# Kernel tuning notes

Hardware: AMD Instinct MI355X
Metric: run time of the kernel (lower is better)

## Reference

```python
import jax, jax.numpy as jnp
import numpy as np

CUTOFF = 5.0

def cubic_cutoff(d):
    # f(0)=1, f(y)=0, smooth first derivatives at both ends
    y = CUTOFF
    xc = 1.0 - 1.5 * (d * d) / (y * y) + 0.5 * (d * d * d) / (y * y * y)
    return jnp.where(d <= 0.0, 1.0, jnp.where(d >= y, 0.0, xc))


def setup_inputs() -> dict:
    key = jax.random.key(0)
    ks = jax.random.split(key, 16)
    B, N, H = 64, 64, 128
    h = jax.random.normal(ks[0], (B, N, H), jnp.float32)
    x = jax.random.uniform(ks[1], (B, N, 3), jnp.float32) * 10.0  # 10A box -> partial neighbor sparsity
    node_mask = jnp.ones((B, N), dtype=bool)
    h0 = jax.random.normal(ks[2], (B, N, H), jnp.float32)
    s = lambda fin: 1.0 / np.sqrt(fin)
    # edge_mlp: Linear(2H+1 -> H), SiLU, Linear(H -> H), SiLU
    We1 = jax.random.normal(ks[3], (2 * H + 1, H), jnp.float32) * s(2 * H + 1)
    be1 = jnp.zeros((H,), jnp.float32)
    We2 = jax.random.normal(ks[4], (H, H), jnp.float32) * s(H)
    be2 = jnp.zeros((H,), jnp.float32)
    # node_mlp: Linear(H + residual_nf + H = 3H -> H), SiLU, Linear(H -> H)
    Wn1 = jax.random.normal(ks[5], (3 * H, H), jnp.float32) * s(3 * H)
    bn1 = jnp.zeros((H,), jnp.float32)
    Wn2 = jax.random.normal(ks[6], (H, H), jnp.float32) * s(H)
    bn2 = jnp.zeros((H,), jnp.float32)
    # coord_mlp: Linear(H -> H), SiLU, Linear(H -> 1, no bias, xavier gain=0.001)
    Wc1 = jax.random.normal(ks[7], (H, H), jnp.float32) * s(H)
    bc1 = jnp.zeros((H,), jnp.float32)
    Wc2 = jax.random.normal(ks[8], (H, 1), jnp.float32) * (0.001 * s(H))
    return {"h": h, "x": x, "node_mask": node_mask, "h0": h0,
            "We1": We1, "be1": be1, "We2": We2, "be2": be2,
            "Wn1": Wn1, "bn1": bn1, "Wn2": Wn2, "bn2": bn2,
            "Wc1": Wc1, "bc1": bc1, "Wc2": Wc2}


def reference(h, x, node_mask, h0, We1, be1, We2, be2, Wn1, bn1, Wn2, bn2, Wc1, bc1, Wc2):
    B, N, H = h.shape
    # pairwise distances; distances are detached in the torch default path
    diff = x[:, :, None, :] - x[:, None, :, :]                     # [B,N,N,3]
    d = jax.lax.stop_gradient(jnp.sqrt(jnp.sum(diff * diff, -1)))  # [B,N,N]
    eye = jnp.eye(N, dtype=bool)[None]
    mask = (node_mask[:, :, None] & node_mask[:, None, :]
            & (d < CUTOFF) & (~eye))                               # [B,N,N]
    maskf = mask.astype(h.dtype)
    # edge model: feat[b,j,k] = [h[b,j], h[b,k], d^2]
    feat = jnp.concatenate([
        jnp.broadcast_to(h[:, :, None, :], (B, N, N, H)),
        jnp.broadcast_to(h[:, None, :, :], (B, N, N, H)),
        (d * d)[..., None]], axis=-1)                              # [B,N,N,2H+1]
    e = jax.nn.silu(feat @ We1 + be1)
    e = jax.nn.silu(e @ We2 + be2)
    mij = e * (cubic_cutoff(d) * maskf)[..., None]                 # [B,N,N,H]
    # node model: sum messages into receiver j
    mi = jnp.sum(mij, axis=2)                                      # [B,N,H]
    nfeat = jnp.concatenate([h, mi, h0], axis=-1)                  # [B,N,3H]
    h_out = jax.nn.silu(nfeat @ Wn1 + bn1) @ Wn2 + bn2
    h_new = h + h_out                                              # recurrent
    # coord model (scatter-add semantics of the intended math)
    phi = jax.nn.silu(mij @ Wc1 + bc1) @ Wc2                       # [B,N,N,1]
    C = 1.0 / (N - 1.0)
    x_up = C * jnp.sum(diff * phi * maskf[..., None], axis=2)      # [B,N,3]
    x_new = jnp.clip(x + x_up, -1000.0, 1000.0)
    return (h_new, x_new)
```

## Files before the change

kernel.cpp:

```cpp
#include <hip/hip_runtime.h>

#define Hh 128
#define Nn 64
#define CAP 2048
#define TPB 16

typedef _Float16 f16x8 __attribute__((ext_vector_type(8)));
typedef float f32x4 __attribute__((ext_vector_type(4)));
typedef unsigned int u32;

__device__ __forceinline__ float silu_f(float v){
    return v * __builtin_amdgcn_rcpf(1.0f + __expf(-v));
}
__device__ __forceinline__ int swz(int row, int cb){ return row*256 + (cb ^ ((row & 7) << 4)); }

#define WT_BYTES (9*32768)

__global__ __launch_bounds__(256) void k_wp(
    const float* __restrict__ x,
    const float* __restrict__ We1, const float* __restrict__ We2, const float* __restrict__ Wc1,
    const float* __restrict__ Wn1, const float* __restrict__ Wn2, char* __restrict__ wT,
    u32* __restrict__ cntB, u32* __restrict__ off_g, u32* __restrict__ cnt_g,
    u32* __restrict__ code_g, float* __restrict__ d2_g, float* __restrict__ cut_g)
{
    const int tid = threadIdx.x;
    if (blockIdx.x >= 64){
        if (blockIdx.x == 128){
            if (tid < 16){
                f16x8 v;
                #pragma unroll
                for (int i=0;i<8;i++) v[i] = (_Float16)We1[256*Hh + tid*8 + i];
                *(f16x8*)(wT + 8*32768 + tid*16) = v;
            }
            return;
        }
        const int id  = (blockIdx.x-64)*256 + tid;
        const int mat = id >> 11;
        const int r   = id & 2047;
        const int n   = r >> 4;
        const int kg  = r & 15;
        const float* __restrict__ src;
        int koff = 0;
        switch (mat){
            case 0: src = We2; break;
            case 1: src = Wc1; break;
            case 2: src = Wn1; break;
            case 3: src = Wn1; koff = 128; break;
            case 4: src = Wn1; koff = 256; break;
            case 5: src = Wn2; break;
            case 6: src = We1; break;
            default: src = We1; koff = 128; break;
        }
        f16x8 v;
        #pragma unroll
        for (int i=0;i<8;i++) v[i] = (_Float16)src[(koff + kg*8 + i)*Hh + n];
        *(f16x8*)(wT + mat*32768 + n*256 + kg*16) = v;
        return;
    }

    __shared__ float sX[192];
    __shared__ int sCnt[64], sOff[64];
    const int b  = blockIdx.x;
    const int wd = tid >> 6;
    const int l  = tid & 63;

    if (tid < 192) sX[tid] = x[b*192 + tid];
    __syncthreads();

    for (int jj = 0; jj < 16; jj++){
        const int j = wd*16 + jj;
        const float dx0 = sX[j*3+0]-sX[l*3+0];
        const float dx1 = sX[j*3+1]-sX[l*3+1];
        const float dx2 = sX[j*3+2]-sX[l*3+2];
        const float d2 = dx0*dx0 + dx1*dx1 + dx2*dx2;
        const bool valid = (l != j) && (d2 < 25.0f);
        const unsigned long long bal = __ballot(valid);
        if (l == 0) sCnt[j] = (int)__popcll(bal);
    }
    __syncthreads();
    if (tid < 64){
        int v = sCnt[tid];
        int incl = v;
        #pragma unroll
        for (int off=1; off<64; off<<=1){
            int o = __shfl_up(incl, off);
            if (l >= off) incl += o;
        }
        sOff[tid] = incl - v;
    }
    __syncthreads();
    if (tid < 64){
        off_g[b*64 + tid] = (u32)sOff[tid];
        cnt_g[b*64 + tid] = (u32)sCnt[tid];
        if (tid == 63){
            int tot = sOff[63] + sCnt[63];
            cntB[b] = (u32)(tot > CAP ? CAP : tot);
        }
    }
    for (int jj = 0; jj < 16; jj++){
        const int j = wd*16 + jj;
        const float dx0 = sX[j*3+0]-sX[l*3+0];
        const float dx1 = sX[j*3+1]-sX[l*3+1];
        const float dx2 = sX[j*3+2]-sX[l*3+2];
        const float d2 = dx0*dx0 + dx1*dx1 + dx2*dx2;
        const bool valid = (l != j) && (d2 < 25.0f);
        const unsigned long long bal = __ballot(valid);
        const int pos = __popcll(bal & ((1ull << l) - 1ull));
        if (valid){
            const int dst = sOff[j] + pos;
            if (dst < CAP){
                const int e = b*CAP + dst;
                code_g[e] = (u32)((j << 6) | l);
                d2_g[e]   = d2;
                cut_g[e]  = 1.0f - 0.06f*d2 + 0.004f*d2*sqrtf(d2);
            }
        }
    }
}

__global__ __launch_bounds__(256, 2) void k_preG(
    const float* __restrict__ h, const char* __restrict__ wT, const float* __restrict__ be1,
    _Float16* __restrict__ Aout, _Float16* __restrict__ Bout)
{
    __shared__ __align__(16) char sA[4096];

    const int r0  = blockIdx.x * 16;
    const int tid = threadIdx.x;
    const int w   = tid >> 6;
    const int l   = tid & 63;
    const int lrow= l & 15;
    const int lk  = l >> 4;
    const int n0 = 2*w, n1 = n0 + 1;
    const int colA = n0*16 + lrow, colB = n1*16 + lrow;

    {
        const int row = tid >> 4;
        const int g   = tid & 15;
        const float4* src = (const float4*)(h + (r0+row)*Hh + g*8);
        const float4 v0 = src[0], v1 = src[1];
        f16x8 e;
        e[0]=(_Float16)v0.x; e[1]=(_Float16)v0.y; e[2]=(_Float16)v0.z; e[3]=(_Float16)v0.w;
        e[4]=(_Float16)v1.x; e[5]=(_Float16)v1.y; e[6]=(_Float16)v1.z; e[7]=(_Float16)v1.w;
        *(f16x8*)(sA + swz(row, g*16)) = e;
    }
    __syncthreads();

    const char* WaT = wT + 6*32768;
    const char* WbT = wT + 7*32768;

    f32x4 accA[2], accB[2];
    {
        const float ba = be1[colA], bb = be1[colB];
        accA[0] = (f32x4){ba,ba,ba,ba};
        accA[1] = (f32x4){bb,bb,bb,bb};
        accB[0] = (f32x4){0.f,0.f,0.f,0.f};
        accB[1] = (f32x4){0.f,0.f,0.f,0.f};
    }
    #pragma unroll
    for (int kb=0;kb<4;kb++){
        const int cb = kb*64 + lk*16;
        const f16x8 a   = *(const f16x8*)(sA  + swz(lrow, cb));
        const f16x8 bA0 = *(const f16x8*)(WaT + (n0*16+lrow)*256 + cb);
        const f16x8 bA1 = *(const f16x8*)(WaT + (n1*16+lrow)*256 + cb);
        const f16x8 bB0 = *(const f16x8*)(WbT + (n0*16+lrow)*256 + cb);
        const f16x8 bB1 = *(const f16x8*)(WbT + (n1*16+lrow)*256 + cb);
        accA[0] = __builtin_amdgcn_mfma_f32_16x16x32_f16(a, bA0, accA[0], 0, 0, 0);
        accA[1] = __builtin_amdgcn_mfma_f32_16x16x32_f16(a, bA1, accA[1], 0, 0, 0);
        accB[0] = __builtin_amdgcn_mfma_f32_16x16x32_f16(a, bB0, accB[0], 0, 0, 0);
        accB[1] = __builtin_amdgcn_mfma_f32_16x16x32_f16(a, bB1, accB[1], 0, 0, 0);
    }
    #pragma unroll
    for (int r=0;r<4;r++){
        const int row = r0 + lk*4 + r;
        Aout[row*Hh + colA] = (_Float16)accA[0][r];
        Aout[row*Hh + colB] = (_Float16)accA[1][r];
        Bout[row*Hh + colA] = (_Float16)accB[0][r];
        Bout[row*Hh + colB] = (_Float16)accB[1][r];
    }
}

__global__ __launch_bounds__(256, 2) void k_edge(
    const _Float16* __restrict__ Ain, const _Float16* __restrict__ Bin,
    const char* __restrict__ wT,
    const float* __restrict__ be2_g, const float* __restrict__ bc1_g, const float* __restrict__ Wc2,
    const u32* __restrict__ cntB, const u32* __restrict__ code_g,
    const float* __restrict__ d2_g, const float* __restrict__ cut_g,
    float* __restrict__ mi_p, float* __restrict__ phi_g)
{
    __shared__ __align__(16) char sE1[32768];
    __shared__ __align__(16) char sM[32768];
    __shared__ int   sBj[128];
    __shared__ u32   sCode[128];
    __shared__ float sD2[128], sCut[128];
    __shared__ float sPhP[4][128];

    const int bid = blockIdx.x;
    const int b   = bid & 63;
    const int t   = bid >> 6;
    const int E_b = (int)cntB[b];
    const int r0  = t*128;
    if (r0 >= E_b) return;
    const int R   = (E_b - r0 < 128) ? (E_b - r0) : 128;
    const int MT  = (R + 15) >> 4;

    const int tid = threadIdx.x;
    const int w   = tid >> 6;
    const int l   = tid & 63;
    const int lrow= l & 15;
    const int lk  = l >> 4;
    const int n0 = 2*w, n1 = n0 + 1;
    const int colA = n0*16 + lrow, colB = n1*16 + lrow;
    const char* We2T = wT;
    const char* Wc1T = wT + 32768;

    if (tid < 128){
        if (tid < R){
            const u32 c = code_g[b*CAP + r0 + tid];
            sCode[tid] = c;
            sBj[tid]   = (int)(c >> 6);
            sD2[tid]   = d2_g[b*CAP + r0 + tid];
            sCut[tid]  = cut_g[b*CAP + r0 + tid];
        } else {
            sCode[tid] = 0; sBj[tid] = -1; sD2[tid] = 0.f; sCut[tid] = 0.f;
        }
    }
    __syncthreads();

    {
        const f16x8* W6 = (const f16x8*)(wT + 8*32768);
        #pragma unroll
        for (int pass=0; pass<2; pass++){
            const int row = pass*64 + (tid >> 2);
            if (row < MT*16){
                const int q = tid & 3;
                const u32 c = sCode[row];
                const int jl = (int)(c >> 6), kl = (int)(c & 63);
                const _Float16 d2h = (_Float16)sD2[row];
                f16x8 dsplat;
                #pragma unroll
                for (int i=0;i<8;i++) dsplat[i] = d2h;
                const f16x8* Aj = (const f16x8*)(Ain + (b*Nn+jl)*Hh + q*32);
                const f16x8* Bk = (const f16x8*)(Bin + (b*Nn+kl)*Hh + q*32);
                #pragma unroll
                for (int s=0;s<4;s++){
                    f16x8 pre = Aj[s] + Bk[s] + W6[q*4+s]*dsplat;
                    f16x8 e;
                    #pragma unroll
                    for (int i=0;i<8;i++) e[i] = (_Float16)silu_f((float)pre[i]);
                    *(f16x8*)(sE1 + swz(row, q*64 + s*16)) = e;
                }
            }
        }
    }
    __syncthreads();

    f32x4 acc[4][2];
    for (int tb = 0; tb < MT; tb += 4){
        const int MTp = (MT - tb < 4) ? (MT - tb) : 4;
        {
            const float b2a = be2_g[colA], b2b = be2_g[colB];
            #pragma unroll
            for (int mt=0;mt<4;mt++){
                acc[mt][0] = (f32x4){b2a,b2a,b2a,b2a};
                acc[mt][1] = (f32x4){b2b,b2b,b2b,b2b};
            }
        }
        #pragma unroll
        for (int kb=0;kb<4;kb++){
            const int cb = kb*64 + lk*16;
            const f16x8 bA = *(const f16x8*)(We2T + (n0*16+lrow)*256 + cb);
            const f16x8 bB = *(const f16x8*)(We2T + (n1*16+lrow)*256 + cb);
            #pragma unroll
            for (int mt=0;mt<4;mt++){
                if (mt < MTp){
                    const f16x8 a = *(const f16x8*)(sE1 + swz((tb+mt)*16 + lrow, cb));
                    acc[mt][0] = __builtin_amdgcn_mfma_f32_16x16x32_f16(a, bA, acc[mt][0], 0, 0, 0);
                    acc[mt][1] = __builtin_amdgcn_mfma_f32_16x16x32_f16(a, bB, acc[mt][1], 0, 0, 0);
                }
            }
        }
        #pragma unroll
        for (int mt=0;mt<4;mt++){
            if (mt < MTp){
                #pragma unroll
                for (int r=0;r<4;r++){
                    const int row = (tb+mt)*16 + lk*4 + r;
                    const float m0 = silu_f(acc[mt][0][r]) * sCut[row];
                    const float m1 = silu_f(acc[mt][1][r]) * sCut[row];
                    const int xr  = (row & 7) << 4;
                    *(_Float16*)(sM + row*256 + ((colA*2) ^ xr)) = (_Float16)m0;
                    *(_Float16*)(sM + row*256 + ((colB*2) ^ xr)) = (_Float16)m1;
                }
            }
        }
    }
    __syncthreads();

    for (int tb = 0; tb < MT; tb += 4){
        const int MTp = (MT - tb < 4) ? (MT - tb) : 4;
        {
            const float c1a = bc1_g[colA], c1b = bc1_g[colB];
            #pragma unroll
            for (int mt=0;mt<4;mt++){
                acc[mt][0] = (f32x4){c1a,c1a,c1a,c1a};
                acc[mt][1] = (f32x4){c1b,c1b,c1b,c1b};
            }
        }
        #pragma unroll
        for (int kb=0;kb<4;kb++){
            const int cb = kb*64 + lk*16;
            const f16x8 bA = *(const f16x8*)(Wc1T + (n0*16+lrow)*256 + cb);
            const f16x8 bB = *(const f16x8*)(Wc1T + (n1*16+lrow)*256 + cb);
            #pragma unroll
            for (int mt=0;mt<4;mt++){
                if (mt < MTp){
                    const f16x8 a = *(const f16x8*)(sM + swz((tb+mt)*16 + lrow, cb));
                    acc[mt][0] = __builtin_amdgcn_mfma_f32_16x16x32_f16(a, bA, acc[mt][0], 0, 0, 0);
                    acc[mt][1] = __builtin_amdgcn_mfma_f32_16x16x32_f16(a, bB, acc[mt][1], 0, 0, 0);
                }
            }
        }
        const float wca = Wc2[colA], wcb = Wc2[colB];
        float php[16];
        #pragma unroll
        for (int mt=0;mt<4;mt++){
            if (mt < MTp){
                #pragma unroll
                for (int r=0;r<4;r++)
                    php[mt*4+r] = silu_f(acc[mt][0][r])*wca + silu_f(acc[mt][1][r])*wcb;
            }
        }
        #pragma unroll
        for (int i=0;i<16;i++){
            if ((i>>2) < MTp){
                php[i] += __shfl_xor(php[i], 1);
                php[i] += __shfl_xor(php[i], 2);
                php[i] += __shfl_xor(php[i], 4);
                php[i] += __shfl_xor(php[i], 8);
            }
        }
        if (lrow == 0){
            #pragma unroll
            for (int mt=0;mt<4;mt++){
                if (mt < MTp){
                    #pragma unroll
                    for (int r=0;r<4;r++)
                        sPhP[w][(tb+mt)*16 + lk*4 + r] = php[mt*4+r];
                }
            }
        }
    }

    {
        const int col  = tid & 127;
        const int half = tid >> 7;
        const int slot = (t & 1)*2 + half;
        float sum = 0.f;
        int cur = -1;
        const int rbeg = half*64, rend = rbeg + 64;
        for (int r = rbeg; r < rend; ++r){
            const int bj = sBj[r];
            const float m = (float)(*(const _Float16*)(sM + r*256 + ((col*2) ^ ((r&7)<<4))));
            if (bj != cur){
                if (cur >= 0) mi_p[((size_t)slot*4096 + (b<<6) + cur)*128 + col] = sum;
                cur = bj; sum = 0.f;
            }
            sum += m;
        }
        if (cur >= 0) mi_p[((size_t)slot*4096 + (b<<6) + cur)*128 + col] = sum;
    }
    __syncthreads();

    if (tid < 128 && tid < R){
        const float phi = sPhP[0][tid] + sPhP[1][tid] + sPhP[2][tid] + sPhP[3][tid];
        phi_g[b*CAP + r0 + tid] = phi;
    }
}

__global__ __launch_bounds__(256) void k_reduce(
    const float* __restrict__ x,
    const u32* __restrict__ off_g, const u32* __restrict__ cnt_g,
    const u32* __restrict__ code_g, const float* __restrict__ phi_g,
    const float* __restrict__ mi_p,
    _Float16* __restrict__ mi_g, float* __restrict__ out_x)
{
    const int tid = threadIdx.x;
    const int wd  = tid >> 6;
    const int l   = tid & 63;
    const int gid = blockIdx.x*4 + wd;
    const int b   = gid >> 6;

    const int cnt = (int)cnt_g[gid];
    const int off = (int)off_g[gid];

    bool v0=false, v1=false, v2=false, v3=false;
    if (cnt > 0){
        const int t0 = off >> 7;
        const int t1 = (off + cnt - 1) >> 7;
        {
            const int s0 = off - t0*128;
            const int e0 = ((off+cnt) < (t0+1)*128 ? (off+cnt) : (t0+1)*128) - t0*128;
            const bool h0 = (s0 < 64), h1 = (e0 > 64);
            if ((t0 & 1) == 0){ v0 |= h0; v1 |= h1; } else { v2 |= h0; v3 |= h1; }
        }
        if (t1 != t0){
            const int e0 = (off + cnt) - t1*128;
            const bool h0 = true, h1 = (e0 > 64);
            if ((t1 & 1) == 0){ v0 |= h0; v1 |= h1; } else { v2 |= h0; v3 |= h1; }
        }
    }

    #pragma unroll
    for (int p=0;p<2;p++){
        const int col = l*2 + p;
        const size_t base = (size_t)gid*128 + col;
        float s = 0.f;
        if (v0) s += mi_p[base];
        if (v1) s += mi_p[(size_t)4096*128 + base];
        if (v2) s += mi_p[(size_t)2*4096*128 + base];
        if (v3) s += mi_p[(size_t)3*4096*128 + base];
        mi_g[gid*Hh + col] = (_Float16)s;
    }

    float w0=0.f, w1=0.f, w2=0.f;
    if (l < cnt && (off + l) < CAP){
        const int e = b*CAP + off + l;
        const int kl = (int)(code_g[e] & 63);
        const float phi = phi_g[e];
        w0 = (x[gid*3+0] - x[(b*Nn+kl)*3+0]) * phi;
        w1 = (x[gid*3+1] - x[(b*Nn+kl)*3+1]) * phi;
        w2 = (x[gid*3+2] - x[(b*Nn+kl)*3+2]) * phi;
    }
    #pragma unroll
    for (int off2=1; off2<64; off2<<=1){
        w0 += __shfl_xor(w0, off2);
        w1 += __shfl_xor(w1, off2);
        w2 += __shfl_xor(w2, off2);
    }
    if (l == 0){
        const float C = 1.0f/63.0f;
        out_x[gid*3+0] = fminf(fmaxf(x[gid*3+0] + C*w0, -1000.f), 1000.f);
        out_x[gid*3+1] = fminf(fmaxf(x[gid*3+1] + C*w1, -1000.f), 1000.f);
        out_x[gid*3+2] = fminf(fmaxf(x[gid*3+2] + C*w2, -1000.f), 1000.f);
    }
}

__global__ __launch_bounds__(256, 2) void k_node(
    const float* __restrict__ h, const _Float16* __restrict__ mi_g,
    const float* __restrict__ h0,
    const char* __restrict__ wT,
    const float* __restrict__ bn1_g, const float* __restrict__ bn2_g,
    float* __restrict__ out_h)
{
    __shared__ __align__(16) char sA[8192];
    __shared__ __align__(16) char sHid[8192];

    const int r0  = blockIdx.x * 32;
    const int tid = threadIdx.x;
    const int w   = tid >> 6;
    const int l   = tid & 63;
    const int lrow= l & 15;
    const int lk  = l >> 4;
    const int n0 = 2*w, n1 = n0 + 1;
    const int colA = n0*16 + lrow, colB = n1*16 + lrow;

    f32x4 acc[2][2];
    {
        const float b1a = bn1_g[colA], b1b = bn1_g[colB];
        acc[0][0] = (f32x4){b1a,b1a,b1a,b1a};
        acc[0][1] = (f32x4){b1b,b1b,b1b,b1b};
        acc[1][0] = (f32x4){b1a,b1a,b1a,b1a};
        acc[1][1] = (f32x4){b1b,b1b,b1b,b1b};
    }

    const int arow = tid >> 3;
    const int g    = tid & 7;

    for (int c = 0; c < 3; c++){
        if (c == 1){
            const f16x8* src = (const f16x8*)(mi_g + (r0+arow)*Hh + g*16);
            *(f16x8*)(sA + swz(arow, g*32))      = src[0];
            *(f16x8*)(sA + swz(arow, g*32+16))   = src[1];
        } else {
            const float* base = (c == 0) ? h : h0;
            const float4* src = (const float4*)(base + (r0+arow)*Hh + g*16);
            const float4 v0=src[0], v1=src[1], v2=src[2], v3=src[3];
            f16x8 e0, e1;
            e0[0]=(_Float16)v0.x; e0[1]=(_Float16)v0.y; e0[2]=(_Float16)v0.z; e0[3]=(_Float16)v0.w;
            e0[4]=(_Float16)v1.x; e0[5]=(_Float16)v1.y; e0[6]=(_Float16)v1.z; e0[7]=(_Float16)v1.w;
            e1[0]=(_Float16)v2.x; e1[1]=(_Float16)v2.y; e1[2]=(_Float16)v2.z; e1[3]=(_Float16)v2.w;
            e1[4]=(_Float16)v3.x; e1[5]=(_Float16)v3.y; e1[6]=(_Float16)v3.z; e1[7]=(_Float16)v3.w;
            *(f16x8*)(sA + swz(arow, g*32))    = e0;
            *(f16x8*)(sA + swz(arow, g*32+16)) = e1;
        }
        __syncthreads();
        const char* Wimg = wT + (2+c)*32768;
        #pragma unroll
        for (int kb=0;kb<4;kb++){
            const int cb = kb*64 + lk*16;
            const f16x8 bA = *(const f16x8*)(Wimg + (n0*16+lrow)*256 + cb);
            const f16x8 bB = *(const f16x8*)(Wimg + (n1*16+lrow)*256 + cb);
            #pragma unroll
            for (int mt=0;mt<2;mt++){
                const f16x8 a = *(const f16x8*)(sA + swz(mt*16 + lrow, cb));
                acc[mt][0] = __builtin_amdgcn_mfma_f32_16x16x32_f16(a, bA, acc[mt][0], 0, 0, 0);
                acc[mt][1] = __builtin_amdgcn_mfma_f32_16x16x32_f16(a, bB, acc[mt][1], 0, 0, 0);
            }
        }
        __syncthreads();
    }

    #pragma unroll
    for (int mt=0;mt<2;mt++){
        #pragma unroll
        for (int r=0;r<4;r++){
            const int row = mt*16 + lk*4 + r;
            const int xr  = (row & 7) << 4;
            *(_Float16*)(sHid + row*256 + ((colA*2) ^ xr)) = (_Float16)silu_f(acc[mt][0][r]);
            *(_Float16*)(sHid + row*256 + ((colB*2) ^ xr)) = (_Float16)silu_f(acc[mt][1][r]);
        }
    }
    __syncthreads();

    const char* Wn2T = wT + 5*32768;
    f32x4 acc2[2][2];
    {
        const float b2a = bn2_g[colA], b2b = bn2_g[colB];
        acc2[0][0] = (f32x4){b2a,b2a,b2a,b2a};
        acc2[0][1] = (f32x4){b2b,b2b,b2b,b2b};
        acc2[1][0] = (f32x4){b2a,b2a,b2a,b2a};
        acc2[1][1] = (f32x4){b2b,b2b,b2b,b2b};
    }
    #pragma unroll
    for (int kb=0;kb<4;kb++){
        const int cb = kb*64 + lk*16;
        const f16x8 bA = *(const f16x8*)(Wn2T + (n0*16+lrow)*256 + cb);
        const f16x8 bB = *(const f16x8*)(Wn2T + (n1*16+lrow)*256 + cb);
        #pragma unroll
        for (int mt=0;mt<2;mt++){
            const f16x8 a = *(const f16x8*)(sHid + swz(mt*16 + lrow, cb));
            acc2[mt][0] = __builtin_amdgcn_mfma_f32_16x16x32_f16(a, bA, acc2[mt][0], 0, 0, 0);
            acc2[mt][1] = __builtin_amdgcn_mfma_f32_16x16x32_f16(a, bB, acc2[mt][1], 0, 0, 0);
        }
    }
    #pragma unroll
    for (int mt=0;mt<2;mt++){
        #pragma unroll
        for (int r=0;r<4;r++){
            const int row = r0 + mt*16 + lk*4 + r;
            out_h[row*Hh + colA] = h[row*Hh + colA] + acc2[mt][0][r];
            out_h[row*Hh + colB] = h[row*Hh + colB] + acc2[mt][1][r];
        }
    }
}

extern "C" void kernel_launch(void* const* d_in, const int* in_sizes, int n_in,
                              void* d_out, int out_size, void* d_ws, size_t ws_size,
                              hipStream_t stream) {
    const float* h   = (const float*)d_in[0];
    const float* x   = (const float*)d_in[1];
    const float* h0  = (const float*)d_in[3];
    const float* We1 = (const float*)d_in[4];
    const float* be1 = (const float*)d_in[5];
    const float* We2 = (const float*)d_in[6];
    const float* be2 = (const float*)d_in[7];
    const float* Wn1 = (const float*)d_in[8];
    const float* bn1 = (const float*)d_in[9];
    const float* Wn2 = (const float*)d_in[10];
    const float* bn2 = (const float*)d_in[11];
    const float* Wc1 = (const float*)d_in[12];
    const float* bc1 = (const float*)d_in[13];
    const float* Wc2 = (const float*)d_in[14];

    float* out_h = (float*)d_out;
    float* out_x = out_h + 64*64*128;

    char*      wT   = (char*)d_ws;
    _Float16*  A    = (_Float16*)(wT + WT_BYTES);
    _Float16*  Bv   = A + 4096*128;
    _Float16*  mi   = Bv + 4096*128;
    u32*       cntB = (u32*)(mi + 4096*128);
    u32*       offg = cntB + 64;
    u32*       cntg = offg + 4096;
    u32*       code = cntg + 4096;
    float*     d2g  = (float*)(code + 64*CAP);
    float*     cutg = d2g + 64*CAP;
    float*     phig = cutg + 64*CAP;
    float*     mip  = phig + 64*CAP;

    k_wp    <<<129, 256, 0, stream>>>(x, We1, We2, Wc1, Wn1, Wn2, wT,
                                      cntB, offg, cntg, code, d2g, cutg);
    k_preG  <<<256, 256, 0, stream>>>(h, wT, be1, A, Bv);
    k_edge  <<<64*TPB, 256, 0, stream>>>(A, Bv, wT, be2, bc1, Wc2,
                                         cntB, code, d2g, cutg, mip, phig);
    k_reduce<<<1024, 256, 0, stream>>>(x, offg, cntg, code, phig, mip, mi, out_x);
    k_node  <<<128, 256, 0, stream>>>(h, mi, h0, wT, bn1, bn2, out_h);
}
```

Measured before the change: 83.57 us.

## Drop reduce kernel: fold coord update into edge, partial sums into node

The k_reduce launch is removed. The edge kernel now computes per-receiver coordinate partial sums directly from stored dx vectors and phi. The node kernel merges the mi partials and x_up partials using a slot mask. Edge tiles shrink from 128 to 64 rows with twice as many blocks, which raises parallelism and halves shared memory per block. This saves one launch and the phi round trip, at the cost of extra global reads of fp32 partials inside k_node.

```diff
diff --git a/kernel.cpp b/kernel.cpp
--- a/kernel.cpp
+++ b/kernel.cpp
@@ -3,7 +3,7 @@
 #define Hh 128
 #define Nn 64
 #define CAP 2048
-#define TPB 16
+#define TPB 32
 
 typedef _Float16 f16x8 __attribute__((ext_vector_type(8)));
 typedef float f32x4 __attribute__((ext_vector_type(4)));
@@ -13,6 +13,25 @@
     return v * __builtin_amdgcn_rcpf(1.0f + __expf(-v));
 }
 __device__ __forceinline__ int swz(int row, int cb){ return row*256 + (cb ^ ((row & 7) << 4)); }
+
+__device__ __forceinline__ int slot_mask(int off, int cnt){
+    if (cnt <= 0) return 0;
+    const int t0 = off >> 6, t1 = (off + cnt - 1) >> 6;
+    const int s0 = off & 63;
+    const int lim = (t0 + 1) << 6;
+    const int end0 = ((off + cnt) < lim ? (off + cnt) : lim) - (t0 << 6);
+    int m = 0;
+    const int p0 = (t0 & 1) * 2;
+    if (s0 < 32)   m |= 1 << p0;
+    if (end0 > 32) m |= 1 << (p0 + 1);
+    if (t1 != t0){
+        const int e1 = (off + cnt) - (t1 << 6);
+        const int p1 = (t1 & 1) * 2;
+        m |= 1 << p1;
+        if (e1 > 32) m |= 1 << (p1 + 1);
+    }
+    return m;
+}
 
 #define WT_BYTES (9*32768)
 
@@ -21,7 +40,7 @@
     const float* __restrict__ We1, const float* __restrict__ We2, const float* __restrict__ Wc1,
     const float* __restrict__ Wn1, const float* __restrict__ Wn2, char* __restrict__ wT,
     u32* __restrict__ cntB, u32* __restrict__ off_g, u32* __restrict__ cnt_g,
-    u32* __restrict__ code_g, float* __restrict__ d2_g, float* __restrict__ cut_g)
+    u32* __restrict__ code_g, float4* __restrict__ dx_g, float* __restrict__ cut_g)
 {
     const int tid = threadIdx.x;
     if (blockIdx.x >= 64){
@@ -111,7 +130,7 @@
             if (dst < CAP){
                 const int e = b*CAP + dst;
                 code_g[e] = (u32)((j << 6) | l);
-                d2_g[e]   = d2;
+                dx_g[e]   = (float4){dx0, dx1, dx2, d2};
                 cut_g[e]  = 1.0f - 0.06f*d2 + 0.004f*d2*sqrtf(d2);
             }
         }
@@ -184,23 +203,24 @@
     const char* __restrict__ wT,
     const float* __restrict__ be2_g, const float* __restrict__ bc1_g, const float* __restrict__ Wc2,
     const u32* __restrict__ cntB, const u32* __restrict__ code_g,
-    const float* __restrict__ d2_g, const float* __restrict__ cut_g,
-    float* __restrict__ mi_p, float* __restrict__ phi_g)
+    const float4* __restrict__ dx_g, const float* __restrict__ cut_g,
+    float* __restrict__ mi_p, float* __restrict__ xup_p)
 {
-    __shared__ __align__(16) char sE1[32768];
-    __shared__ __align__(16) char sM[32768];
-    __shared__ int   sBj[128];
-    __shared__ u32   sCode[128];
-    __shared__ float sD2[128], sCut[128];
-    __shared__ float sPhP[4][128];
+    __shared__ __align__(16) char sE1[16384];
+    __shared__ __align__(16) char sM[16384];
+    __shared__ int    sBj[64];
+    __shared__ u32    sCode[64];
+    __shared__ float4 sDxD[64];
+    __shared__ float  sCut[64];
+    __shared__ float  sPhP[4][64];
 
     const int bid = blockIdx.x;
     const int b   = bid & 63;
     const int t   = bid >> 6;
     const int E_b = (int)cntB[b];
-    const int r0  = t*128;
+    const int r0  = t*64;
     if (r0 >= E_b) return;
-    const int R   = (E_b - r0 < 128) ? (E_b - r0) : 128;
+    const int R   = (E_b - r0 < 64) ? (E_b - r0) : 64;
     const int MT  = (R + 15) >> 4;
 
     const int tid = threadIdx.x;
@@ -213,57 +233,53 @@
     const char* We2T = wT;
     const char* Wc1T = wT + 32768;
 
-    if (tid < 128){
+    if (tid < 64){
         if (tid < R){
             const u32 c = code_g[b*CAP + r0 + tid];
             sCode[tid] = c;
             sBj[tid]   = (int)(c >> 6);
-            sD2[tid]   = d2_g[b*CAP + r0 + tid];
+            sDxD[tid]  = dx_g[b*CAP + r0 + tid];
             sCut[tid]  = cut_g[b*CAP + r0 + tid];
         } else {
-            sCode[tid] = 0; sBj[tid] = -1; sD2[tid] = 0.f; sCut[tid] = 0.f;
+            sCode[tid] = 0; sBj[tid] = -1;
+            sDxD[tid]  = (float4){0.f,0.f,0.f,0.f};
+            sCut[tid]  = 0.f;
         }
     }
     __syncthreads();
 
     {
         const f16x8* W6 = (const f16x8*)(wT + 8*32768);
-        #pragma unroll
-        for (int pass=0; pass<2; pass++){
-            const int row = pass*64 + (tid >> 2);
-            if (row < MT*16){
-                const int q = tid & 3;
-                const u32 c = sCode[row];
-                const int jl = (int)(c >> 6), kl = (int)(c & 63);
-                const _Float16 d2h = (_Float16)sD2[row];
-                f16x8 dsplat;
+        const int row = tid >> 2;
+        if (row < MT*16){
+            const int q = tid & 3;
+            const u32 c = sCode[row];
+            const int jl = (int)(c >> 6), kl = (int)(c & 63);
+            const _Float16 d2h = (_Float16)sDxD[row].w;
+            f16x8 dsplat;
+            #pragma unroll
+            for (int i=0;i<8;i++) dsplat[i] = d2h;
+            const f16x8* Aj = (const f16x8*)(Ain + (b*Nn+jl)*Hh + q*32);
+            const f16x8* Bk = (const f16x8*)(Bin + (b*Nn+kl)*Hh + q*32);
+            #pragma unroll
+            for (int s=0;s<4;s++){
+                f16x8 pre = Aj[s] + Bk[s] + W6[q*4+s]*dsplat;
+                f16x8 e;
                 #pragma unroll
-                for (int i=0;i<8;i++) dsplat[i] = d2h;
-                const f16x8* Aj = (const f16x8*)(Ain + (b*Nn+jl)*Hh + q*32);
-                const f16x8* Bk = (const f16x8*)(Bin + (b*Nn+kl)*Hh + q*32);
-                #pragma unroll
-                for (int s=0;s<4;s++){
-                    f16x8 pre = Aj[s] + Bk[s] + W6[q*4+s]*dsplat;
-                    f16x8 e;
-                    #pragma unroll
-                    for (int i=0;i<8;i++) e[i] = (_Float16)silu_f((float)pre[i]);
-                    *(f16x8*)(sE1 + swz(row, q*64 + s*16)) = e;
-                }
+                for (int i=0;i<8;i++) e[i] = (_Float16)silu_f((float)pre[i]);
+                *(f16x8*)(sE1 + swz(row, q*64 + s*16)) = e;
             }
         }
     }
     __syncthreads();
 
     f32x4 acc[4][2];
-    for (int tb = 0; tb < MT; tb += 4){
-        const int MTp = (MT - tb < 4) ? (MT - tb) : 4;
-        {
-            const float b2a = be2_g[colA], b2b = be2_g[colB];
-            #pragma unroll
-            for (int mt=0;mt<4;mt++){
-                acc[mt][0] = (f32x4){b2a,b2a,b2a,b2a};
-                acc[mt][1] = (f32x4){b2b,b2b,b2b,b2b};
-            }
+    {
+        const float b2a = be2_g[colA], b2b = be2_g[colB];
+        #pragma unroll
+        for (int mt=0;mt<4;mt++){
+            acc[mt][0] = (f32x4){b2a,b2a,b2a,b2a};
+            acc[mt][1] = (f32x4){b2b,b2b,b2b,b2b};
         }
         #pragma unroll
         for (int kb=0;kb<4;kb++){
@@ -272,8 +288,8 @@
             const f16x8 bB = *(const f16x8*)(We2T + (n1*16+lrow)*256 + cb);
             #pragma unroll
             for (int mt=0;mt<4;mt++){
-                if (mt < MTp){
-                    const f16x8 a = *(const f16x8*)(sE1 + swz((tb+mt)*16 + lrow, cb));
+                if (mt < MT){
+                    const f16x8 a = *(const f16x8*)(sE1 + swz(mt*16 + lrow, cb));
                     acc[mt][0] = __builtin_amdgcn_mfma_f32_16x16x32_f16(a, bA, acc[mt][0], 0, 0, 0);
                     acc[mt][1] = __builtin_amdgcn_mfma_f32_16x16x32_f16(a, bB, acc[mt][1], 0, 0, 0);
                 }
@@ -281,10 +297,10 @@
         }
         #pragma unroll
         for (int mt=0;mt<4;mt++){
-            if (mt < MTp){
+            if (mt < MT){
                 #pragma unroll
                 for (int r=0;r<4;r++){
-                    const int row = (tb+mt)*16 + lk*4 + r;
+                    const int row = mt*16 + lk*4 + r;
                     const float m0 = silu_f(acc[mt][0][r]) * sCut[row];
                     const float m1 = silu_f(acc[mt][1][r]) * sCut[row];
                     const int xr  = (row & 7) << 4;
@@ -296,15 +312,12 @@
     }
     __syncthreads();
 
-    for (int tb = 0; tb < MT; tb += 4){
-        const int MTp = (MT - tb < 4) ? (MT - tb) : 4;
-        {
-            const float c1a = bc1_g[colA], c1b = bc1_g[colB];
-            #pragma unroll
-            for (int mt=0;mt<4;mt++){
-                acc[mt][0] = (f32x4){c1a,c1a,c1a,c1a};
-                acc[mt][1] = (f32x4){c1b,c1b,c1b,c1b};
-            }
+    {
+        const float c1a = bc1_g[colA], c1b = bc1_g[colB];
+        #pragma unroll
+        for (int mt=0;mt<4;mt++){
+            acc[mt][0] = (f32x4){c1a,c1a,c1a,c1a};
+            acc[mt][1] = (f32x4){c1b,c1b,c1b,c1b};
         }
         #pragma unroll
         for (int kb=0;kb<4;kb++){
@@ -313,8 +326,8 @@
             const f16x8 bB = *(const f16x8*)(Wc1T + (n1*16+lrow)*256 + cb);
             #pragma unroll
             for (int mt=0;mt<4;mt++){
-                if (mt < MTp){
-                    const f16x8 a = *(const f16x8*)(sM + swz((tb+mt)*16 + lrow, cb));
+                if (mt < MT){
+                    const f16x8 a = *(const f16x8*)(sM + swz(mt*16 + lrow, cb));
                     acc[mt][0] = __builtin_amdgcn_mfma_f32_16x16x32_f16(a, bA, acc[mt][0], 0, 0, 0);
                     acc[mt][1] = __builtin_amdgcn_mfma_f32_16x16x32_f16(a, bB, acc[mt][1], 0, 0, 0);
                 }
@@ -324,7 +337,7 @@
         float php[16];
         #pragma unroll
         for (int mt=0;mt<4;mt++){
-            if (mt < MTp){
+            if (mt < MT){
                 #pragma unroll
                 for (int r=0;r<4;r++)
                     php[mt*4+r] = silu_f(acc[mt][0][r])*wca + silu_f(acc[mt][1][r])*wcb;
@@ -332,7 +345,7 @@
         }
         #pragma unroll
         for (int i=0;i<16;i++){
-            if ((i>>2) < MTp){
+            if ((i>>2) < MT){
                 php[i] += __shfl_xor(php[i], 1);
                 php[i] += __shfl_xor(php[i], 2);
                 php[i] += __shfl_xor(php[i], 4);
@@ -342,10 +355,10 @@
         if (lrow == 0){
             #pragma unroll
             for (int mt=0;mt<4;mt++){
-                if (mt < MTp){
+                if (mt < MT){
                     #pragma unroll
                     for (int r=0;r<4;r++)
-                        sPhP[w][(tb+mt)*16 + lk*4 + r] = php[mt*4+r];
+                        sPhP[w][mt*16 + lk*4 + r] = php[mt*4+r];
                 }
             }
         }
@@ -357,7 +370,7 @@
         const int slot = (t & 1)*2 + half;
         float sum = 0.f;
         int cur = -1;
-        const int rbeg = half*64, rend = rbeg + 64;
+        const int rbeg = half*32, rend = rbeg + 32;
         for (int r = rbeg; r < rend; ++r){
             const int bj = sBj[r];
             const float m = (float)(*(const _Float16*)(sM + r*256 + ((col*2) ^ ((r&7)<<4))));
@@ -371,86 +384,35 @@
     }
     __syncthreads();
 
-    if (tid < 128 && tid < R){
-        const float phi = sPhP[0][tid] + sPhP[1][tid] + sPhP[2][tid] + sPhP[3][tid];
-        phi_g[b*CAP + r0 + tid] = phi;
-    }
-}
-
-__global__ __launch_bounds__(256) void k_reduce(
-    const float* __restrict__ x,
-    const u32* __restrict__ off_g, const u32* __restrict__ cnt_g,
-    const u32* __restrict__ code_g, const float* __restrict__ phi_g,
-    const float* __restrict__ mi_p,
-    _Float16* __restrict__ mi_g, float* __restrict__ out_x)
-{
-    const int tid = threadIdx.x;
-    const int wd  = tid >> 6;
-    const int l   = tid & 63;
-    const int gid = blockIdx.x*4 + wd;
-    const int b   = gid >> 6;
-
-    const int cnt = (int)cnt_g[gid];
-    const int off = (int)off_g[gid];
-
-    bool v0=false, v1=false, v2=false, v3=false;
-    if (cnt > 0){
-        const int t0 = off >> 7;
-        const int t1 = (off + cnt - 1) >> 7;
-        {
-            const int s0 = off - t0*128;
-            const int e0 = ((off+cnt) < (t0+1)*128 ? (off+cnt) : (t0+1)*128) - t0*128;
-            const bool h0 = (s0 < 64), h1 = (e0 > 64);
-            if ((t0 & 1) == 0){ v0 |= h0; v1 |= h1; } else { v2 |= h0; v3 |= h1; }
-        }
-        if (t1 != t0){
-            const int e0 = (off + cnt) - t1*128;
-            const bool h0 = true, h1 = (e0 > 64);
-            if ((t1 & 1) == 0){ v0 |= h0; v1 |= h1; } else { v2 |= h0; v3 |= h1; }
-        }
-    }
-
-    #pragma unroll
-    for (int p=0;p<2;p++){
-        const int col = l*2 + p;
-        const size_t base = (size_t)gid*128 + col;
-        float s = 0.f;
-        if (v0) s += mi_p[base];
-        if (v1) s += mi_p[(size_t)4096*128 + base];
-        if (v2) s += mi_p[(size_t)2*4096*128 + base];
-        if (v3) s += mi_p[(size_t)3*4096*128 + base];
-        mi_g[gid*Hh + col] = (_Float16)s;
-    }
-
-    float w0=0.f, w1=0.f, w2=0.f;
-    if (l < cnt && (off + l) < CAP){
-        const int e = b*CAP + off + l;
-        const int kl = (int)(code_g[e] & 63);
-        const float phi = phi_g[e];
-        w0 = (x[gid*3+0] - x[(b*Nn+kl)*3+0]) * phi;
-        w1 = (x[gid*3+1] - x[(b*Nn+kl)*3+1]) * phi;
-        w2 = (x[gid*3+2] - x[(b*Nn+kl)*3+2]) * phi;
-    }
-    #pragma unroll
-    for (int off2=1; off2<64; off2<<=1){
-        w0 += __shfl_xor(w0, off2);
-        w1 += __shfl_xor(w1, off2);
-        w2 += __shfl_xor(w2, off2);
-    }
-    if (l == 0){
-        const float C = 1.0f/63.0f;
-        out_x[gid*3+0] = fminf(fmaxf(x[gid*3+0] + C*w0, -1000.f), 1000.f);
-        out_x[gid*3+1] = fminf(fmaxf(x[gid*3+1] + C*w1, -1000.f), 1000.f);
-        out_x[gid*3+2] = fminf(fmaxf(x[gid*3+2] + C*w2, -1000.f), 1000.f);
+    if (tid < 6){
+        const int c    = tid % 3;
+        const int half = tid / 3;
+        const int slot = (t & 1)*2 + half;
+        float sum = 0.f;
+        int cur = -1;
+        const int rbeg = half*32, rend = rbeg + 32;
+        for (int r = rbeg; r < rend; ++r){
+            const int bj = sBj[r];
+            const float phi = sPhP[0][r] + sPhP[1][r] + sPhP[2][r] + sPhP[3][r];
+            const float4 dd = sDxD[r];
+            const float dx = (c==0) ? dd.x : ((c==1) ? dd.y : dd.z);
+            if (bj != cur){
+                if (cur >= 0) xup_p[((size_t)slot*4096 + (b<<6) + cur)*4 + c] = sum;
+                cur = bj; sum = 0.f;
+            }
+            sum += phi * dx;
+        }
+        if (cur >= 0) xup_p[((size_t)slot*4096 + (b<<6) + cur)*4 + c] = sum;
     }
 }
 
 __global__ __launch_bounds__(256, 2) void k_node(
-    const float* __restrict__ h, const _Float16* __restrict__ mi_g,
-    const float* __restrict__ h0,
+    const float* __restrict__ h, const float* __restrict__ h0,
     const char* __restrict__ wT,
     const float* __restrict__ bn1_g, const float* __restrict__ bn2_g,
-    float* __restrict__ out_h)
+    const float* __restrict__ mi_p, const u32* __restrict__ off_g, const u32* __restrict__ cnt_g,
+    const float* __restrict__ xup_p, const float* __restrict__ x,
+    float* __restrict__ out_h, float* __restrict__ out_x)
 {
     __shared__ __align__(16) char sA[8192];
     __shared__ __align__(16) char sHid[8192];
@@ -464,6 +426,20 @@
     const int n0 = 2*w, n1 = n0 + 1;
     const int colA = n0*16 + lrow, colB = n1*16 + lrow;
 
+    if (tid < 96){
+        const int row = tid / 3;
+        const int c   = tid - row*3;
+        const int gid = r0 + row;
+        const int vm  = slot_mask((int)off_g[gid], (int)cnt_g[gid]);
+        float s = 0.f;
+        if (vm & 1) s += xup_p[((size_t)0*4096 + gid)*4 + c];
+        if (vm & 2) s += xup_p[((size_t)1*4096 + gid)*4 + c];
+        if (vm & 4) s += xup_p[((size_t)2*4096 + gid)*4 + c];
+        if (vm & 8) s += xup_p[((size_t)3*4096 + gid)*4 + c];
+        const float xv = x[gid*3 + c] + (1.0f/63.0f)*s;
+        out_x[gid*3 + c] = fminf(fmaxf(xv, -1000.f), 1000.f);
+    }
+
     f32x4 acc[2][2];
     {
         const float b1a = bn1_g[colA], b1b = bn1_g[colB];
@@ -478,9 +454,27 @@
 
     for (int c = 0; c < 3; c++){
         if (c == 1){
-            const f16x8* src = (const f16x8*)(mi_g + (r0+arow)*Hh + g*16);
-            *(f16x8*)(sA + swz(arow, g*32))      = src[0];
-            *(f16x8*)(sA + swz(arow, g*32+16))   = src[1];
+            const int gid = r0 + arow;
+            const int vm  = slot_mask((int)off_g[gid], (int)cnt_g[gid]);
+            float4 s0 = {0,0,0,0}, s1 = {0,0,0,0}, s2 = {0,0,0,0}, s3 = {0,0,0,0};
+            #pragma unroll
+            for (int slot=0; slot<4; slot++){
+                if (vm & (1<<slot)){
+                    const float4* mp = (const float4*)(mi_p + ((size_t)slot*4096 + gid)*128 + g*16);
+                    const float4 a0=mp[0], a1=mp[1], a2=mp[2], a3=mp[3];
+                    s0.x+=a0.x; s0.y+=a0.y; s0.z+=a0.z; s0.w+=a0.w;
+                    s1.x+=a1.x; s1.y+=a1.y; s1.z+=a1.z; s1.w+=a1.w;
+                    s2.x+=a2.x; s2.y+=a2.y; s2.z+=a2.z; s2.w+=a2.w;
+                    s3.x+=a3.x; s3.y+=a3.y; s3.z+=a3.z; s3.w+=a3.w;
+                }
+            }
+            f16x8 e0, e1;
+            e0[0]=(_Float16)s0.x; e0[1]=(_Float16)s0.y; e0[2]=(_Float16)s0.z; e0[3]=(_Float16)s0.w;
+            e0[4]=(_Float16)s1.x; e0[5]=(_Float16)s1.y; e0[6]=(_Float16)s1.z; e0[7]=(_Float16)s1.w;
+            e1[0]=(_Float16)s2.x; e1[1]=(_Float16)s2.y; e1[2]=(_Float16)s2.z; e1[3]=(_Float16)s2.w;
+            e1[4]=(_Float16)s3.x; e1[5]=(_Float16)s3.y; e1[6]=(_Float16)s3.z; e1[7]=(_Float16)s3.w;
+            *(f16x8*)(sA + swz(arow, g*32))    = e0;
+            *(f16x8*)(sA + swz(arow, g*32+16)) = e1;
         } else {
             const float* base = (c == 0) ? h : h0;
             const float4* src = (const float4*)(base + (r0+arow)*Hh + g*16);
@@ -578,21 +572,20 @@
     char*      wT   = (char*)d_ws;
     _Float16*  A    = (_Float16*)(wT + WT_BYTES);
     _Float16*  Bv   = A + 4096*128;
-    _Float16*  mi   = Bv + 4096*128;
-    u32*       cntB = (u32*)(mi + 4096*128);
+    float4*    dxg  = (float4*)(Bv + 4096*128);
+    float*     cutg = (float*)(dxg + 64*CAP);
+    u32*       cntB = (u32*)(cutg + 64*CAP);
     u32*       offg = cntB + 64;
     u32*       cntg = offg + 4096;
     u32*       code = cntg + 4096;
-    float*     d2g  = (float*)(code + 64*CAP);
-    float*     cutg = d2g + 64*CAP;
-    float*     phig = cutg + 64*CAP;
-    float*     mip  = phig + 64*CAP;
-
-    k_wp    <<<129, 256, 0, stream>>>(x, We1, We2, Wc1, Wn1, Wn2, wT,
-                                      cntB, offg, cntg, code, d2g, cutg);
-    k_preG  <<<256, 256, 0, stream>>>(h, wT, be1, A, Bv);
-    k_edge  <<<64*TPB, 256, 0, stream>>>(A, Bv, wT, be2, bc1, Wc2,
-                                         cntB, code, d2g, cutg, mip, phig);
-    k_reduce<<<1024, 256, 0, stream>>>(x, offg, cntg, code, phig, mip, mi, out_x);
-    k_node  <<<128, 256, 0, stream>>>(h, mi, h0, wT, bn1, bn2, out_h);
-}
+    float*     mip  = (float*)(code + 64*CAP);
+    float*     xupp = mip + (size_t)4*4096*128;
+
+    k_wp  <<<129, 256, 0, stream>>>(x, We1, We2, Wc1, Wn1, Wn2, wT,
+                                    cntB, offg, cntg, code, dxg, cutg);
+    k_preG<<<256, 256, 0, stream>>>(h, wT, be1, A, Bv);
+    k_edge<<<64*TPB, 256, 0, stream>>>(A, Bv, wT, be2, bc1, Wc2,
+                                       cntB, code, dxg, cutg, mip, xupp);
+    k_node<<<128, 256, 0, stream>>>(h, h0, wT, bn1, bn2,
+                                    mip, offg, cntg, xupp, x, out_h, out_x);
+}
```

Result: faster. 81.73 us (median of 2 runs) (-2.2%).
